# Performance work log

Hardware: AMD Instinct MI355X
Metric: run time of the kernel (lower is better)

## Reference

```python
import jax, jax.numpy as jnp
import numpy as np

NUM_HEADS = 8
GN_GROUPS = 8
GN_EPS = 1e-5


def setup_inputs() -> dict:
    key = jax.random.key(0)
    k1, k2, k3 = jax.random.split(key, 3)
    B, C, H, W = 8, 512, 32, 32
    x = jax.random.normal(k1, (B, C, H, W), dtype=jnp.float32)
    w_qkv = jax.random.normal(k2, (3 * C, C), dtype=jnp.float32) * 0.02
    w_proj = jax.random.normal(k3, (C, C), dtype=jnp.float32) * 0.02
    gamma = jnp.ones((C,), dtype=jnp.float32)
    beta = jnp.zeros((C,), dtype=jnp.float32)
    return {"x": x, "w_qkv": w_qkv, "w_proj": w_proj, "gamma": gamma, "beta": beta}


def reference(x, w_qkv, w_proj, gamma, beta):
    B, C, H, W = x.shape
    nh = NUM_HEADS
    hd = C // nh
    N = H * W
    scale = jnp.asarray(hd, x.dtype) ** -0.5

    xf = x.reshape(B, C, N)                                  # [B,C,N]
    # 1x1 conv (no bias) == channel matmul
    qkv = jnp.einsum('oc,bcn->bon', w_qkv, xf)               # [B,3C,N]
    qkv = qkv.reshape(B, 3, nh, hd, N)
    q, k, v = qkv[:, 0], qkv[:, 1], qkv[:, 2]                # [B,h,d,N]

    attn = jnp.einsum('bhdn,bhdm->bhnm', q, k) * scale       # [B,h,N,N]
    attn = jax.nn.softmax(attn, axis=-1)
    out = jnp.einsum('bhnm,bhdm->bhdn', attn, v)             # [B,h,d,N]
    out = out.reshape(B, C, N)

    out = jnp.einsum('oc,bcn->bon', w_proj, out).reshape(B, C, H, W)

    # GroupNorm(8, C)
    g = GN_GROUPS
    og = out.reshape(B, g, C // g, H, W)
    mean = og.mean(axis=(2, 3, 4), keepdims=True)
    var = og.var(axis=(2, 3, 4), keepdims=True)
    normed = ((og - mean) * jax.lax.rsqrt(var + GN_EPS)).reshape(B, C, H, W)
    normed = normed * gamma[None, :, None, None] + beta[None, :, None, None]

    return normed + x
```

## Files before the change

### kernel.cpp

```cpp
#include <hip/hip_runtime.h>

#define B_DIM 8
#define GN_EPS 1e-5f

typedef short s16x8 __attribute__((ext_vector_type(8)));
typedef float f32x4 __attribute__((ext_vector_type(4)));
typedef unsigned int u32x2 __attribute__((ext_vector_type(2)));
typedef s16x8 s16x8_a __attribute__((may_alias));
typedef u32x2 u32x2_a __attribute__((may_alias));

__device__ inline unsigned short f2bf(float f) {
    unsigned u = __builtin_bit_cast(unsigned, f);
    u += 0x7fffu + ((u >> 16) & 1u);
    return (unsigned short)(u >> 16);
}

__device__ inline unsigned cvtpk(float lo, float hi) {
    unsigned r;
    asm("v_cvt_pk_bf16_f32 %0, %1, %2" : "=v"(r) : "v"(lo), "v"(hi));
    return r;
}

__device__ inline f32x4 mfma16(s16x8 a, s16x8 b, f32x4 c) {
    return __builtin_amdgcn_mfma_f32_16x16x32_bf16(a, b, c, 0, 0, 0);
}

__device__ inline void gload16(const unsigned short* g, unsigned short* l) {
    __builtin_amdgcn_global_load_lds(
        (const __attribute__((address_space(1))) unsigned int*)g,
        (__attribute__((address_space(3))) unsigned int*)l, 16, 0, 0);
}

#define SWZ(r, c) ((r)*64 + ((c) ^ (((r)&7) << 3)))

__global__ __launch_bounds__(256)
void wcvt_kernel(const float4* __restrict__ src, unsigned short* __restrict__ dst) {
    int idx = blockIdx.x * 256 + threadIdx.x;
    float4 v = src[idx];
    ushort4 pk;
    pk.x = f2bf(v.x); pk.y = f2bf(v.y); pk.z = f2bf(v.z); pk.w = f2bf(v.w);
    *(ushort4*)&dst[(size_t)idx * 4] = pk;
}

__global__ __launch_bounds__(256)
void xT_kernel(const float* __restrict__ x, unsigned short* __restrict__ xt) {
    const int ntile = blockIdx.x, ctile = blockIdx.y, b = blockIdx.z;
    const int t = threadIdx.x;
    __shared__ float ts[64][65];
    const float* xp = x + ((size_t)b * 512 + ctile * 64) * 1024 + ntile * 64;
    #pragma unroll
    for (int i = 0; i < 16; ++i) {
        int f = i * 256 + t; int c = f >> 6, n = f & 63;
        ts[n][c] = xp[(size_t)c * 1024 + n];
    }
    __syncthreads();
    unsigned short* xo = xt + ((size_t)b * 1024 + ntile * 64) * 512 + ctile * 64;
    #pragma unroll
    for (int i = 0; i < 16; ++i) {
        int f = i * 256 + t; int n = f >> 6, c = f & 63;
        xo[(size_t)n * 512 + c] = f2bf(ts[n][c]);
    }
}

template<int O_DIM, int MODE>
__global__ __launch_bounds__(256)
void mm_kernel(const unsigned short* __restrict__ Wb,
               const unsigned short* __restrict__ Xt,
               float* __restrict__ Yout,
               unsigned short* __restrict__ qt,
               unsigned short* __restrict__ kt,
               unsigned short* __restrict__ vt) {
    constexpr int OT = O_DIM / 128;
    const int bi = blockIdx.x;
    const int nt = bi & 7;
    const int rest = bi >> 3;
    const int ot = rest % OT;
    const int b  = rest / OT;

    const int t = threadIdx.x;
    const int w = t >> 6, lid = t & 63, lr = lid & 15, g4 = lid >> 4;
    const int wr = w >> 1, wc = w & 1;

    __shared__ unsigned short lds[17408];
    unsigned short* Ws = lds;
    unsigned short* Xs = lds + 4096;

    const unsigned short* wsrc = Wb + ((size_t)(ot * 128 + w * 32 + (lid >> 2))) * 512 + (lid & 3) * 8;
    const unsigned short* xsrc = Xt + ((size_t)b * 1024 + nt * 128 + w * 32 + (lid >> 2)) * 512 + (lid & 3) * 8;
    unsigned short* wdst0 = Ws + (w * 32) * 32;
    unsigned short* wdst1 = Ws + (w * 32 + 16) * 32;
    unsigned short* xdst0 = Xs + (w * 32) * 32;
    unsigned short* xdst1 = Xs + (w * 32 + 16) * 32;

    const f32x4 Z4 = {0.f, 0.f, 0.f, 0.f};
    f32x4 acc[4][4];
    #pragma unroll
    for (int i = 0; i < 4; ++i)
        #pragma unroll
        for (int j = 0; j < 4; ++j) acc[i][j] = Z4;

    #pragma unroll 1
    for (int k0 = 0; k0 < 512; k0 += 32) {
        __syncthreads();
        gload16(wsrc + k0, wdst0);
        gload16(wsrc + k0 + 16 * 512, wdst1);
        gload16(xsrc + k0, xdst0);
        gload16(xsrc + k0 + 16 * 512, xdst1);
        __syncthreads();
        s16x8 av[4], bv[4];
        #pragma unroll
        for (int mi = 0; mi < 4; ++mi)
            av[mi] = *(const s16x8*)&Ws[(wr * 64 + mi * 16 + lr) * 32 + g4 * 8];
        #pragma unroll
        for (int nj = 0; nj < 4; ++nj)
            bv[nj] = *(const s16x8*)&Xs[(wc * 64 + nj * 16 + lr) * 32 + g4 * 8];
        #pragma unroll
        for (int mi = 0; mi < 4; ++mi)
            #pragma unroll
            for (int nj = 0; nj < 4; ++nj)
                acc[mi][nj] = mfma16(av[mi], bv[nj], acc[mi][nj]);
    }

    if (MODE == 0) {
        float* yp = Yout + ((size_t)b * O_DIM + ot * 128 + wr * 64) * 1024 + nt * 128 + wc * 64;
        #pragma unroll
        for (int mi = 0; mi < 4; ++mi)
            #pragma unroll
            for (int nj = 0; nj < 4; ++nj)
                #pragma unroll
                for (int r = 0; r < 4; ++r)
                    yp[(size_t)(mi * 16 + g4 * 4 + r) * 1024 + nj * 16 + lr] = acc[mi][nj][r];
    } else {
        __syncthreads();
        unsigned short* T = lds + w * 4352;
        const int obase = ot * 128 + wr * 64;
        const int s = obase >> 9;
        const int h = (obase >> 6) & 7;
        const float scl = (s == 0) ? 0.18033688f : 1.0f;
        #pragma unroll
        for (int mi = 0; mi < 4; ++mi)
            #pragma unroll
            for (int nj = 0; nj < 4; ++nj)
                #pragma unroll
                for (int r = 0; r < 4; ++r) {
                    int ol = mi * 16 + g4 * 4 + r, nl = nj * 16 + lr;
                    unsigned short v = f2bf(acc[mi][nj][r] * scl);
                    T[(s < 2) ? (nl * 68 + ol) : (ol * 68 + nl)] = v;
                }
        const size_t n0w = (size_t)nt * 128 + wc * 64;
        const int row = (lid >> 5), j = lid & 31;
        if (s < 2) {
            unsigned short* q = (s == 0) ? qt : kt;
            unsigned int* dst = (unsigned int*)(q + (((size_t)b * 8 + h) * 1024 + n0w) * 64);
            #pragma unroll
            for (int p = 0; p < 32; ++p) {
                int rw = p * 2 + row;
                unsigned int lo = T[rw * 68 + 2 * j];
                unsigned int hi = T[rw * 68 + 2 * j + 1];
                dst[(size_t)rw * 32 + j] = lo | (hi << 16);
            }
        } else {
            unsigned int* dst = (unsigned int*)(vt + ((size_t)b * 8 + h) * 65536 + n0w);
            #pragma unroll
            for (int p = 0; p < 32; ++p) {
                int rw = p * 2 + row;
                unsigned int lo = T[rw * 68 + 2 * j];
                unsigned int hi = T[rw * 68 + 2 * j + 1];
                dst[(size_t)rw * 512 + j] = lo | (hi << 16);
            }
        }
    }
}

__global__ __launch_bounds__(256)
void attn_kernel(const unsigned short* __restrict__ qt,
                 const unsigned short* __restrict__ kt,
                 const unsigned short* __restrict__ vt,
                 unsigned short* __restrict__ aout) {
    const int bi = blockIdx.x;
    const int h = bi & 7;
    const int qtile = (bi >> 3) & 7;
    const int b = bi >> 6;

    const int t = threadIdx.x;
    const int w = t >> 6, lid = t & 63, lr = lid & 15, g4 = lid >> 4;
    const int rr = lid >> 3, cc = lid & 7;
    const int csw = (cc ^ rr) << 3;

    __shared__ unsigned short lds[24576];
    unsigned short* Ps = lds + 16384;

    const unsigned short* qbh = qt + ((size_t)b * 8 + h) * 65536;
    const unsigned short* kbh = kt + ((size_t)b * 8 + h) * 65536;
    const unsigned short* vbh = vt + ((size_t)b * 8 + h) * 65536;

    s16x8 qa[2][2];
    #pragma unroll
    for (int mi = 0; mi < 2; ++mi)
        #pragma unroll
        for (int ks = 0; ks < 2; ++ks)
            qa[mi][ks] = *(const s16x8*)(qbh +
                (size_t)(qtile * 128 + w * 32 + mi * 16 + lr) * 64 + ks * 32 + g4 * 8);

    {
        unsigned short* Kd = lds + (w * 16) * 64;
        unsigned short* Vd = lds + 8192 + (w * 16) * 64;
        gload16(kbh + (size_t)(w * 16 + rr) * 64 + csw, Kd);
        gload16(kbh + (size_t)(w * 16 + 8 + rr) * 64 + csw, Kd + 512);
        gload16(vbh + (size_t)(w * 16 + rr) * 1024 + csw, Vd);
        gload16(vbh + (size_t)(w * 16 + 8 + rr) * 1024 + csw, Vd + 512);
    }
    __syncthreads();

    const f32x4 Z4 = {0.f, 0.f, 0.f, 0.f};
    f32x4 acc_o[2][4];
    float l_run[2] = {0.f, 0.f};
    #pragma unroll
    for (int mi = 0; mi < 2; ++mi)
        #pragma unroll
        for (int di = 0; di < 4; ++di) acc_o[mi][di] = Z4;

    #pragma unroll 1
    for (int it = 0; it < 16; ++it) {
        const int sel = it & 1;
        unsigned short* Kc = lds + sel * 4096;
        unsigned short* Vc = lds + 8192 + sel * 4096;

        if (it < 15) {
            const int m1 = (it + 1) * 64;
            unsigned short* Kd = lds + (sel ^ 1) * 4096 + (w * 16) * 64;
            unsigned short* Vd = lds + 8192 + (sel ^ 1) * 4096 + (w * 16) * 64;
            gload16(kbh + (size_t)(m1 + w * 16 + rr) * 64 + csw, Kd);
            gload16(kbh + (size_t)(m1 + w * 16 + 8 + rr) * 64 + csw, Kd + 512);
            gload16(vbh + (size_t)(w * 16 + rr) * 1024 + m1 + csw, Vd);
            gload16(vbh + (size_t)(w * 16 + 8 + rr) * 1024 + m1 + csw, Vd + 512);
        }

        f32x4 sc[2][4];
        #pragma unroll
        for (int mi = 0; mi < 2; ++mi)
            #pragma unroll
            for (int mj = 0; mj < 4; ++mj) sc[mi][mj] = Z4;
        #pragma unroll
        for (int ks = 0; ks < 2; ++ks) {
            s16x8 kb[4];
            #pragma unroll
            for (int mj = 0; mj < 4; ++mj)
                kb[mj] = *(const s16x8*)&Kc[SWZ(mj * 16 + lr, ks * 32 + g4 * 8)];
            #pragma unroll
            for (int mi = 0; mi < 2; ++mi)
                #pragma unroll
                for (int mj = 0; mj < 4; ++mj)
                    sc[mi][mj] = mfma16(kb[mj], qa[mi][ks], sc[mi][mj]);
        }

        #pragma unroll
        for (int mi = 0; mi < 2; ++mi) {
            #pragma unroll
            for (int mj = 0; mj < 4; ++mj) {
                float p0 = __builtin_amdgcn_exp2f(sc[mi][mj][0]);
                float p1 = __builtin_amdgcn_exp2f(sc[mi][mj][1]);
                float p2 = __builtin_amdgcn_exp2f(sc[mi][mj][2]);
                float p3 = __builtin_amdgcn_exp2f(sc[mi][mj][3]);
                l_run[mi] += (p0 + p1) + (p2 + p3);
                u32x2 pk;
                pk.x = cvtpk(p0, p1);
                pk.y = cvtpk(p2, p3);
                *(u32x2_a*)&Ps[SWZ(w * 32 + mi * 16 + lr, mj * 16 + g4 * 4)] = pk;
            }
        }

        #pragma unroll
        for (int ks = 0; ks < 2; ++ks) {
            s16x8 pa[2], vb[4];
            #pragma unroll
            for (int mi = 0; mi < 2; ++mi)
                pa[mi] = *(const s16x8_a*)&Ps[SWZ(w * 32 + mi * 16 + lr, ks * 32 + g4 * 8)];
            #pragma unroll
            for (int di = 0; di < 4; ++di)
                vb[di] = *(const s16x8*)&Vc[SWZ(di * 16 + lr, ks * 32 + g4 * 8)];
            #pragma unroll
            for (int mi = 0; mi < 2; ++mi)
                #pragma unroll
                for (int di = 0; di < 4; ++di)
                    acc_o[mi][di] = mfma16(pa[mi], vb[di], acc_o[mi][di]);
        }
        __syncthreads();
    }

    #pragma unroll
    for (int mi = 0; mi < 2; ++mi) {
        float l = l_run[mi];
        l += __shfl_xor(l, 16);
        l += __shfl_xor(l, 32);
        l_run[mi] = 1.f / l;
    }
    #pragma unroll
    for (int mi = 0; mi < 2; ++mi) {
        float inv[4];
        #pragma unroll
        for (int r = 0; r < 4; ++r)
            inv[r] = __shfl(l_run[mi], g4 * 4 + r);
        #pragma unroll
        for (int di = 0; di < 4; ++di)
            #pragma unroll
            for (int r = 0; r < 4; ++r) {
                int n = qtile * 128 + w * 32 + mi * 16 + g4 * 4 + r;
                int c = h * 64 + di * 16 + lr;
                aout[((size_t)b * 1024 + n) * 512 + c] = f2bf(acc_o[mi][di][r] * inv[r]);
            }
    }
}

__global__ __launch_bounds__(256)
void gn_stats_kernel(const float* __restrict__ proj, float* __restrict__ partial) {
    const int s = blockIdx.x;
    const int g = blockIdx.y;
    const int b = blockIdx.z;
    const int t = threadIdx.x;
    const float4* p4 = (const float4*)(proj + ((size_t)b * 512 + (size_t)g * 64) * 1024)
                       + (size_t)s * 2048;
    float sum = 0.f, sq = 0.f;
    #pragma unroll
    for (int r = 0; r < 8; ++r) {
        float4 v = p4[r * 256 + t];
        sum += v.x + v.y + v.z + v.w;
        sq  += v.x * v.x + v.y * v.y + v.z * v.z + v.w * v.w;
    }
    #pragma unroll
    for (int off = 32; off >= 1; off >>= 1) {
        sum += __shfl_down(sum, off);
        sq  += __shfl_down(sq, off);
    }
    __shared__ float rs[4], rq[4];
    if ((t & 63) == 0) { rs[t >> 6] = sum; rq[t >> 6] = sq; }
    __syncthreads();
    if (t == 0) {
        float* pp = partial + ((size_t)(b * 8 + g) * 8 + s) * 2;
        pp[0] = rs[0] + rs[1] + rs[2] + rs[3];
        pp[1] = rq[0] + rq[1] + rq[2] + rq[3];
    }
}

__global__ __launch_bounds__(256)
void gn_apply_kernel(const float* __restrict__ partial, const float* __restrict__ x,
                     const float* __restrict__ gamma, const float* __restrict__ beta,
                     float* __restrict__ out) {
    const int qtr = blockIdx.x;
    const int g = blockIdx.y;
    const int b = blockIdx.z;
    const int t = threadIdx.x;
    const float* pp = partial + (size_t)(b * 8 + g) * 16;
    float sum = 0.f, sq = 0.f;
    #pragma unroll
    for (int s = 0; s < 8; ++s) { sum += pp[s * 2]; sq += pp[s * 2 + 1]; }
    const float mean = sum * (1.f / 65536.f);
    const float var  = sq * (1.f / 65536.f) - mean * mean;
    const float rstd = rsqrtf(var + GN_EPS);
    const size_t base = ((size_t)b * 512 + (size_t)g * 64) * 1024 + (size_t)qtr * 4096;
    const float4* o4 = (const float4*)(out + base);
    const float4* x4 = (const float4*)(x + base);
    float4* w4 = (float4*)(out + base);
    #pragma unroll
    for (int j = 0; j < 4; ++j) {
        int c = g * 64 + qtr * 4 + j;
        float gm = gamma[c], bt = beta[c];
        float4 v  = o4[j * 256 + t];
        float4 xv = x4[j * 256 + t];
        float4 r;
        r.x = (v.x - mean) * rstd * gm + bt + xv.x;
        r.y = (v.y - mean) * rstd * gm + bt + xv.y;
        r.z = (v.z - mean) * rstd * gm + bt + xv.z;
        r.w = (v.w - mean) * rstd * gm + bt + xv.w;
        w4[j * 256 + t] = r;
    }
}

extern "C" void kernel_launch(void* const* d_in, const int* in_sizes, int n_in,
                              void* d_out, int out_size, void* d_ws, size_t ws_size,
                              hipStream_t stream) {
    (void)in_sizes; (void)n_in; (void)out_size; (void)ws_size;
    const float* x      = (const float*)d_in[0];
    const float* w_qkv  = (const float*)d_in[1];
    const float* w_proj = (const float*)d_in[2];
    const float* gamma  = (const float*)d_in[3];
    const float* beta   = (const float*)d_in[4];
    float* out = (float*)d_out;

    unsigned short* qtb  = (unsigned short*)d_ws;
    unsigned short* ktb  = qtb  + 4194304;
    unsigned short* vtb  = ktb  + 4194304;
    unsigned short* aoutb= vtb  + 4194304;
    unsigned short* xtb  = aoutb+ 4194304;
    unsigned short* wqb  = xtb  + 4194304;
    unsigned short* wpb  = wqb  + 786432;
    float* partial = (float*)(wpb + 262144);

    wcvt_kernel<<<768, 256, 0, stream>>>((const float4*)w_qkv, wqb);
    wcvt_kernel<<<256, 256, 0, stream>>>((const float4*)w_proj, wpb);
    xT_kernel<<<dim3(16, 8, B_DIM), 256, 0, stream>>>(x, xtb);
    mm_kernel<1536, 1><<<768, 256, 0, stream>>>(wqb, xtb, nullptr, qtb, ktb, vtb);
    attn_kernel<<<512, 256, 0, stream>>>(qtb, ktb, vtb, aoutb);
    mm_kernel<512, 0><<<256, 256, 0, stream>>>(wpb, aoutb, out, nullptr, nullptr, nullptr);
    gn_stats_kernel<<<dim3(8, 8, B_DIM), 256, 0, stream>>>(out, partial);
    gn_apply_kernel<<<dim3(16, 8, B_DIM), 256, 0, stream>>>(partial, x, gamma, beta, out);
}
```

Baseline: 91.44 us.

## Fuse GroupNorm stats into projection GEMM and halve attention query tile

The projection GEMM epilogue now computes per-wave sums and sums of squares and writes them as partials, so the separate GroupNorm statistics kernel and its re-read of the projection output are removed. The apply kernel now reduces 16 partials per group instead of 8. Separately, the attention kernel processes 64 query rows per block instead of 128, doubling the grid to 1024 blocks and cutting per-wave registers and LDS. The price is that K/V tiles are loaded twice as often per query row.

```diff
diff --git a/kernel.cpp b/kernel.cpp
--- a/kernel.cpp
+++ b/kernel.cpp
@@ -69,7 +69,8 @@
                float* __restrict__ Yout,
                unsigned short* __restrict__ qt,
                unsigned short* __restrict__ kt,
-               unsigned short* __restrict__ vt) {
+               unsigned short* __restrict__ vt,
+               float* __restrict__ partial) {
     constexpr int OT = O_DIM / 128;
     const int bi = blockIdx.x;
     const int nt = bi & 7;
@@ -121,7 +122,7 @@
                 acc[mi][nj] = mfma16(av[mi], bv[nj], acc[mi][nj]);
     }
 
-    if (MODE == 0) {
+    if (MODE == 0 || MODE == 2) {
         float* yp = Yout + ((size_t)b * O_DIM + ot * 128 + wr * 64) * 1024 + nt * 128 + wc * 64;
         #pragma unroll
         for (int mi = 0; mi < 4; ++mi)
@@ -130,6 +131,29 @@
                 #pragma unroll
                 for (int r = 0; r < 4; ++r)
                     yp[(size_t)(mi * 16 + g4 * 4 + r) * 1024 + nj * 16 + lr] = acc[mi][nj][r];
+        if (MODE == 2) {
+            float s1 = 0.f, s2 = 0.f;
+            #pragma unroll
+            for (int mi = 0; mi < 4; ++mi)
+                #pragma unroll
+                for (int nj = 0; nj < 4; ++nj)
+                    #pragma unroll
+                    for (int r = 0; r < 4; ++r) {
+                        float v = acc[mi][nj][r];
+                        s1 += v;
+                        s2 += v * v;
+                    }
+            #pragma unroll
+            for (int off = 1; off <= 32; off <<= 1) {
+                s1 += __shfl_xor(s1, off);
+                s2 += __shfl_xor(s2, off);
+            }
+            if (lid == 0) {
+                float2* pp = (float2*)partial + ((size_t)(b * 8 + ot * 2 + wr) * 16)
+                             + nt * 2 + wc;
+                *pp = make_float2(s1, s2);
+            }
+        }
     } else {
         __syncthreads();
         unsigned short* T = lds + w * 4352;
@@ -179,28 +203,26 @@
                  unsigned short* __restrict__ aout) {
     const int bi = blockIdx.x;
     const int h = bi & 7;
-    const int qtile = (bi >> 3) & 7;
-    const int b = bi >> 6;
+    const int qtile = (bi >> 3) & 15;
+    const int b = bi >> 7;
 
     const int t = threadIdx.x;
     const int w = t >> 6, lid = t & 63, lr = lid & 15, g4 = lid >> 4;
     const int rr = lid >> 3, cc = lid & 7;
     const int csw = (cc ^ rr) << 3;
 
-    __shared__ unsigned short lds[24576];
+    __shared__ unsigned short lds[20480];
     unsigned short* Ps = lds + 16384;
 
     const unsigned short* qbh = qt + ((size_t)b * 8 + h) * 65536;
     const unsigned short* kbh = kt + ((size_t)b * 8 + h) * 65536;
     const unsigned short* vbh = vt + ((size_t)b * 8 + h) * 65536;
 
-    s16x8 qa[2][2];
-    #pragma unroll
-    for (int mi = 0; mi < 2; ++mi)
-        #pragma unroll
-        for (int ks = 0; ks < 2; ++ks)
-            qa[mi][ks] = *(const s16x8*)(qbh +
-                (size_t)(qtile * 128 + w * 32 + mi * 16 + lr) * 64 + ks * 32 + g4 * 8);
+    s16x8 qa[2];
+    #pragma unroll
+    for (int ks = 0; ks < 2; ++ks)
+        qa[ks] = *(const s16x8*)(qbh +
+            (size_t)(qtile * 64 + w * 16 + lr) * 64 + ks * 32 + g4 * 8);
 
     {
         unsigned short* Kd = lds + (w * 16) * 64;
@@ -213,12 +235,10 @@
     __syncthreads();
 
     const f32x4 Z4 = {0.f, 0.f, 0.f, 0.f};
-    f32x4 acc_o[2][4];
-    float l_run[2] = {0.f, 0.f};
-    #pragma unroll
-    for (int mi = 0; mi < 2; ++mi)
-        #pragma unroll
-        for (int di = 0; di < 4; ++di) acc_o[mi][di] = Z4;
+    f32x4 acc_o[4];
+    float l_run = 0.f;
+    #pragma unroll
+    for (int di = 0; di < 4; ++di) acc_o[di] = Z4;
 
     #pragma unroll 1
     for (int it = 0; it < 16; ++it) {
@@ -236,11 +256,9 @@
             gload16(vbh + (size_t)(w * 16 + 8 + rr) * 1024 + m1 + csw, Vd + 512);
         }
 
-        f32x4 sc[2][4];
-        #pragma unroll
-        for (int mi = 0; mi < 2; ++mi)
-            #pragma unroll
-            for (int mj = 0; mj < 4; ++mj) sc[mi][mj] = Z4;
+        f32x4 sc[4];
+        #pragma unroll
+        for (int mj = 0; mj < 4; ++mj) sc[mj] = Z4;
         #pragma unroll
         for (int ks = 0; ks < 2; ++ks) {
             s16x8 kb[4];
@@ -248,98 +266,52 @@
             for (int mj = 0; mj < 4; ++mj)
                 kb[mj] = *(const s16x8*)&Kc[SWZ(mj * 16 + lr, ks * 32 + g4 * 8)];
             #pragma unroll
-            for (int mi = 0; mi < 2; ++mi)
-                #pragma unroll
-                for (int mj = 0; mj < 4; ++mj)
-                    sc[mi][mj] = mfma16(kb[mj], qa[mi][ks], sc[mi][mj]);
-        }
-
-        #pragma unroll
-        for (int mi = 0; mi < 2; ++mi) {
-            #pragma unroll
-            for (int mj = 0; mj < 4; ++mj) {
-                float p0 = __builtin_amdgcn_exp2f(sc[mi][mj][0]);
-                float p1 = __builtin_amdgcn_exp2f(sc[mi][mj][1]);
-                float p2 = __builtin_amdgcn_exp2f(sc[mi][mj][2]);
-                float p3 = __builtin_amdgcn_exp2f(sc[mi][mj][3]);
-                l_run[mi] += (p0 + p1) + (p2 + p3);
-                u32x2 pk;
-                pk.x = cvtpk(p0, p1);
-                pk.y = cvtpk(p2, p3);
-                *(u32x2_a*)&Ps[SWZ(w * 32 + mi * 16 + lr, mj * 16 + g4 * 4)] = pk;
-            }
+            for (int mj = 0; mj < 4; ++mj)
+                sc[mj] = mfma16(kb[mj], qa[ks], sc[mj]);
+        }
+
+        #pragma unroll
+        for (int mj = 0; mj < 4; ++mj) {
+            float p0 = __builtin_amdgcn_exp2f(sc[mj][0]);
+            float p1 = __builtin_amdgcn_exp2f(sc[mj][1]);
+            float p2 = __builtin_amdgcn_exp2f(sc[mj][2]);
+            float p3 = __builtin_amdgcn_exp2f(sc[mj][3]);
+            l_run += (p0 + p1) + (p2 + p3);
+            u32x2 pk;
+            pk.x = cvtpk(p0, p1);
+            pk.y = cvtpk(p2, p3);
+            *(u32x2_a*)&Ps[SWZ(w * 16 + lr, mj * 16 + g4 * 4)] = pk;
         }
 
         #pragma unroll
         for (int ks = 0; ks < 2; ++ks) {
-            s16x8 pa[2], vb[4];
-            #pragma unroll
-            for (int mi = 0; mi < 2; ++mi)
-                pa[mi] = *(const s16x8_a*)&Ps[SWZ(w * 32 + mi * 16 + lr, ks * 32 + g4 * 8)];
+            s16x8 pa, vb[4];
+            pa = *(const s16x8_a*)&Ps[SWZ(w * 16 + lr, ks * 32 + g4 * 8)];
             #pragma unroll
             for (int di = 0; di < 4; ++di)
                 vb[di] = *(const s16x8*)&Vc[SWZ(di * 16 + lr, ks * 32 + g4 * 8)];
             #pragma unroll
-            for (int mi = 0; mi < 2; ++mi)
-                #pragma unroll
-                for (int di = 0; di < 4; ++di)
-                    acc_o[mi][di] = mfma16(pa[mi], vb[di], acc_o[mi][di]);
+            for (int di = 0; di < 4; ++di)
+                acc_o[di] = mfma16(pa, vb[di], acc_o[di]);
         }
         __syncthreads();
     }
 
-    #pragma unroll
-    for (int mi = 0; mi < 2; ++mi) {
-        float l = l_run[mi];
-        l += __shfl_xor(l, 16);
-        l += __shfl_xor(l, 32);
-        l_run[mi] = 1.f / l;
-    }
-    #pragma unroll
-    for (int mi = 0; mi < 2; ++mi) {
-        float inv[4];
-        #pragma unroll
-        for (int r = 0; r < 4; ++r)
-            inv[r] = __shfl(l_run[mi], g4 * 4 + r);
-        #pragma unroll
-        for (int di = 0; di < 4; ++di)
-            #pragma unroll
-            for (int r = 0; r < 4; ++r) {
-                int n = qtile * 128 + w * 32 + mi * 16 + g4 * 4 + r;
-                int c = h * 64 + di * 16 + lr;
-                aout[((size_t)b * 1024 + n) * 512 + c] = f2bf(acc_o[mi][di][r] * inv[r]);
-            }
-    }
-}
-
-__global__ __launch_bounds__(256)
-void gn_stats_kernel(const float* __restrict__ proj, float* __restrict__ partial) {
-    const int s = blockIdx.x;
-    const int g = blockIdx.y;
-    const int b = blockIdx.z;
-    const int t = threadIdx.x;
-    const float4* p4 = (const float4*)(proj + ((size_t)b * 512 + (size_t)g * 64) * 1024)
-                       + (size_t)s * 2048;
-    float sum = 0.f, sq = 0.f;
-    #pragma unroll
-    for (int r = 0; r < 8; ++r) {
-        float4 v = p4[r * 256 + t];
-        sum += v.x + v.y + v.z + v.w;
-        sq  += v.x * v.x + v.y * v.y + v.z * v.z + v.w * v.w;
-    }
-    #pragma unroll
-    for (int off = 32; off >= 1; off >>= 1) {
-        sum += __shfl_down(sum, off);
-        sq  += __shfl_down(sq, off);
-    }
-    __shared__ float rs[4], rq[4];
-    if ((t & 63) == 0) { rs[t >> 6] = sum; rq[t >> 6] = sq; }
-    __syncthreads();
-    if (t == 0) {
-        float* pp = partial + ((size_t)(b * 8 + g) * 8 + s) * 2;
-        pp[0] = rs[0] + rs[1] + rs[2] + rs[3];
-        pp[1] = rq[0] + rq[1] + rq[2] + rq[3];
-    }
+    l_run += __shfl_xor(l_run, 16);
+    l_run += __shfl_xor(l_run, 32);
+    l_run = 1.f / l_run;
+    float inv[4];
+    #pragma unroll
+    for (int r = 0; r < 4; ++r)
+        inv[r] = __shfl(l_run, g4 * 4 + r);
+    #pragma unroll
+    for (int di = 0; di < 4; ++di)
+        #pragma unroll
+        for (int r = 0; r < 4; ++r) {
+            int n = qtile * 64 + w * 16 + g4 * 4 + r;
+            int c = h * 64 + di * 16 + lr;
+            aout[((size_t)b * 1024 + n) * 512 + c] = f2bf(acc_o[di][r] * inv[r]);
+        }
 }
 
 __global__ __launch_bounds__(256)
@@ -350,10 +322,10 @@
     const int g = blockIdx.y;
     const int b = blockIdx.z;
     const int t = threadIdx.x;
-    const float* pp = partial + (size_t)(b * 8 + g) * 16;
+    const float2* pp = (const float2*)partial + (size_t)(b * 8 + g) * 16;
     float sum = 0.f, sq = 0.f;
     #pragma unroll
-    for (int s = 0; s < 8; ++s) { sum += pp[s * 2]; sq += pp[s * 2 + 1]; }
+    for (int s = 0; s < 16; ++s) { sum += pp[s].x; sq += pp[s].y; }
     const float mean = sum * (1.f / 65536.f);
     const float var  = sq * (1.f / 65536.f) - mean * mean;
     const float rstd = rsqrtf(var + GN_EPS);
@@ -399,9 +371,8 @@
     wcvt_kernel<<<768, 256, 0, stream>>>((const float4*)w_qkv, wqb);
     wcvt_kernel<<<256, 256, 0, stream>>>((const float4*)w_proj, wpb);
     xT_kernel<<<dim3(16, 8, B_DIM), 256, 0, stream>>>(x, xtb);
-    mm_kernel<1536, 1><<<768, 256, 0, stream>>>(wqb, xtb, nullptr, qtb, ktb, vtb);
-    attn_kernel<<<512, 256, 0, stream>>>(qtb, ktb, vtb, aoutb);
-    mm_kernel<512, 0><<<256, 256, 0, stream>>>(wpb, aoutb, out, nullptr, nullptr, nullptr);
-    gn_stats_kernel<<<dim3(8, 8, B_DIM), 256, 0, stream>>>(out, partial);
+    mm_kernel<1536, 1><<<768, 256, 0, stream>>>(wqb, xtb, nullptr, qtb, ktb, vtb, nullptr);
+    attn_kernel<<<1024, 256, 0, stream>>>(qtb, ktb, vtb, aoutb);
+    mm_kernel<512, 2><<<256, 256, 0, stream>>>(wpb, aoutb, out, nullptr, nullptr, nullptr, partial);
     gn_apply_kernel<<<dim3(16, 8, B_DIM), 256, 0, stream>>>(partial, x, gamma, beta, out);
 }
```

Measured after the change: 90.83 us. No clear change (-0.7%).

## Double-buffer GEMM K-loop, fuse GroupNorm stats into proj GEMM, pack xT stores

Applied to the files above, without the earlier changes.

The GEMM main loop now double-buffers its LDS tiles, prefetching the next K slice while the current one feeds the MFMAs, which halves the barriers per iteration. The projection GEMM gets a new mode that reduces per-wave sum and sum-of-squares from the accumulators and writes partials, so the separate gn_stats kernel and its re-read of the output are removed. The apply kernel now reads 16 partials per group. The transpose kernel also writes two bf16 values per 32-bit store.

```diff
diff --git a/kernel.cpp b/kernel.cpp
--- a/kernel.cpp
+++ b/kernel.cpp
@@ -56,9 +56,11 @@
     __syncthreads();
     unsigned short* xo = xt + ((size_t)b * 1024 + ntile * 64) * 512 + ctile * 64;
     #pragma unroll
-    for (int i = 0; i < 16; ++i) {
-        int f = i * 256 + t; int n = f >> 6, c = f & 63;
-        xo[(size_t)n * 512 + c] = f2bf(ts[n][c]);
+    for (int i = 0; i < 8; ++i) {
+        int f = i * 512 + t * 2; int n = f >> 6, c = f & 63;
+        unsigned lo = f2bf(ts[n][c]);
+        unsigned hi = f2bf(ts[n][c + 1]);
+        *(unsigned int*)&xo[(size_t)n * 512 + c] = lo | (hi << 16);
     }
 }
 
@@ -69,7 +71,8 @@
                float* __restrict__ Yout,
                unsigned short* __restrict__ qt,
                unsigned short* __restrict__ kt,
-               unsigned short* __restrict__ vt) {
+               unsigned short* __restrict__ vt,
+               float* __restrict__ partial) {
     constexpr int OT = O_DIM / 128;
     const int bi = blockIdx.x;
     const int nt = bi & 7;
@@ -82,15 +85,11 @@
     const int wr = w >> 1, wc = w & 1;
 
     __shared__ unsigned short lds[17408];
-    unsigned short* Ws = lds;
-    unsigned short* Xs = lds + 4096;
 
     const unsigned short* wsrc = Wb + ((size_t)(ot * 128 + w * 32 + (lid >> 2))) * 512 + (lid & 3) * 8;
     const unsigned short* xsrc = Xt + ((size_t)b * 1024 + nt * 128 + w * 32 + (lid >> 2)) * 512 + (lid & 3) * 8;
-    unsigned short* wdst0 = Ws + (w * 32) * 32;
-    unsigned short* wdst1 = Ws + (w * 32 + 16) * 32;
-    unsigned short* xdst0 = Xs + (w * 32) * 32;
-    unsigned short* xdst1 = Xs + (w * 32 + 16) * 32;
+    const int woff0 = (w * 32) * 32;
+    const int woff1 = (w * 32 + 16) * 32;
 
     const f32x4 Z4 = {0.f, 0.f, 0.f, 0.f};
     f32x4 acc[4][4];
@@ -99,29 +98,40 @@
         #pragma unroll
         for (int j = 0; j < 4; ++j) acc[i][j] = Z4;
 
+    gload16(wsrc, lds + woff0);
+    gload16(wsrc + 16 * 512, lds + woff1);
+    gload16(xsrc, lds + 4096 + woff0);
+    gload16(xsrc + 16 * 512, lds + 4096 + woff1);
+    __syncthreads();
+
     #pragma unroll 1
-    for (int k0 = 0; k0 < 512; k0 += 32) {
-        __syncthreads();
-        gload16(wsrc + k0, wdst0);
-        gload16(wsrc + k0 + 16 * 512, wdst1);
-        gload16(xsrc + k0, xdst0);
-        gload16(xsrc + k0 + 16 * 512, xdst1);
-        __syncthreads();
+    for (int it = 0; it < 16; ++it) {
+        const int sel = it & 1;
+        unsigned short* buf = lds + sel * 8192;
+        if (it < 15) {
+            const int k1 = (it + 1) * 32;
+            unsigned short* nb = lds + (sel ^ 1) * 8192;
+            gload16(wsrc + k1, nb + woff0);
+            gload16(wsrc + k1 + 16 * 512, nb + woff1);
+            gload16(xsrc + k1, nb + 4096 + woff0);
+            gload16(xsrc + k1 + 16 * 512, nb + 4096 + woff1);
+        }
         s16x8 av[4], bv[4];
         #pragma unroll
         for (int mi = 0; mi < 4; ++mi)
-            av[mi] = *(const s16x8*)&Ws[(wr * 64 + mi * 16 + lr) * 32 + g4 * 8];
+            av[mi] = *(const s16x8*)&buf[(wr * 64 + mi * 16 + lr) * 32 + g4 * 8];
         #pragma unroll
         for (int nj = 0; nj < 4; ++nj)
-            bv[nj] = *(const s16x8*)&Xs[(wc * 64 + nj * 16 + lr) * 32 + g4 * 8];
+            bv[nj] = *(const s16x8*)&buf[4096 + (wc * 64 + nj * 16 + lr) * 32 + g4 * 8];
         #pragma unroll
         for (int mi = 0; mi < 4; ++mi)
             #pragma unroll
             for (int nj = 0; nj < 4; ++nj)
                 acc[mi][nj] = mfma16(av[mi], bv[nj], acc[mi][nj]);
-    }
-
-    if (MODE == 0) {
+        __syncthreads();
+    }
+
+    if (MODE == 0 || MODE == 2) {
         float* yp = Yout + ((size_t)b * O_DIM + ot * 128 + wr * 64) * 1024 + nt * 128 + wc * 64;
         #pragma unroll
         for (int mi = 0; mi < 4; ++mi)
@@ -130,8 +140,30 @@
                 #pragma unroll
                 for (int r = 0; r < 4; ++r)
                     yp[(size_t)(mi * 16 + g4 * 4 + r) * 1024 + nj * 16 + lr] = acc[mi][nj][r];
+        if (MODE == 2) {
+            float s1 = 0.f, s2 = 0.f;
+            #pragma unroll
+            for (int mi = 0; mi < 4; ++mi)
+                #pragma unroll
+                for (int nj = 0; nj < 4; ++nj)
+                    #pragma unroll
+                    for (int r = 0; r < 4; ++r) {
+                        float v = acc[mi][nj][r];
+                        s1 += v;
+                        s2 += v * v;
+                    }
+            #pragma unroll
+            for (int off = 1; off <= 32; off <<= 1) {
+                s1 += __shfl_xor(s1, off);
+                s2 += __shfl_xor(s2, off);
+            }
+            if (lid == 0) {
+                float2* pp = (float2*)partial + ((size_t)(b * 8 + ot * 2 + wr) * 16)
+                             + nt * 2 + wc;
+                *pp = make_float2(s1, s2);
+            }
+        }
     } else {
-        __syncthreads();
         unsigned short* T = lds + w * 4352;
         const int obase = ot * 128 + wr * 64;
         const int s = obase >> 9;
@@ -313,36 +345,6 @@
 }
 
 __global__ __launch_bounds__(256)
-void gn_stats_kernel(const float* __restrict__ proj, float* __restrict__ partial) {
-    const int s = blockIdx.x;
-    const int g = blockIdx.y;
-    const int b = blockIdx.z;
-    const int t = threadIdx.x;
-    const float4* p4 = (const float4*)(proj + ((size_t)b * 512 + (size_t)g * 64) * 1024)
-                       + (size_t)s * 2048;
-    float sum = 0.f, sq = 0.f;
-    #pragma unroll
-    for (int r = 0; r < 8; ++r) {
-        float4 v = p4[r * 256 + t];
-        sum += v.x + v.y + v.z + v.w;
-        sq  += v.x * v.x + v.y * v.y + v.z * v.z + v.w * v.w;
-    }
-    #pragma unroll
-    for (int off = 32; off >= 1; off >>= 1) {
-        sum += __shfl_down(sum, off);
-        sq  += __shfl_down(sq, off);
-    }
-    __shared__ float rs[4], rq[4];
-    if ((t & 63) == 0) { rs[t >> 6] = sum; rq[t >> 6] = sq; }
-    __syncthreads();
-    if (t == 0) {
-        float* pp = partial + ((size_t)(b * 8 + g) * 8 + s) * 2;
-        pp[0] = rs[0] + rs[1] + rs[2] + rs[3];
-        pp[1] = rq[0] + rq[1] + rq[2] + rq[3];
-    }
-}
-
-__global__ __launch_bounds__(256)
 void gn_apply_kernel(const float* __restrict__ partial, const float* __restrict__ x,
                      const float* __restrict__ gamma, const float* __restrict__ beta,
                      float* __restrict__ out) {
@@ -350,10 +352,10 @@
     const int g = blockIdx.y;
     const int b = blockIdx.z;
     const int t = threadIdx.x;
-    const float* pp = partial + (size_t)(b * 8 + g) * 16;
+    const float2* pp = (const float2*)partial + (size_t)(b * 8 + g) * 16;
     float sum = 0.f, sq = 0.f;
     #pragma unroll
-    for (int s = 0; s < 8; ++s) { sum += pp[s * 2]; sq += pp[s * 2 + 1]; }
+    for (int s = 0; s < 16; ++s) { sum += pp[s].x; sq += pp[s].y; }
     const float mean = sum * (1.f / 65536.f);
     const float var  = sq * (1.f / 65536.f) - mean * mean;
     const float rstd = rsqrtf(var + GN_EPS);
@@ -399,9 +401,8 @@
     wcvt_kernel<<<768, 256, 0, stream>>>((const float4*)w_qkv, wqb);
     wcvt_kernel<<<256, 256, 0, stream>>>((const float4*)w_proj, wpb);
     xT_kernel<<<dim3(16, 8, B_DIM), 256, 0, stream>>>(x, xtb);
-    mm_kernel<1536, 1><<<768, 256, 0, stream>>>(wqb, xtb, nullptr, qtb, ktb, vtb);
+    mm_kernel<1536, 1><<<768, 256, 0, stream>>>(wqb, xtb, nullptr, qtb, ktb, vtb, nullptr);
     attn_kernel<<<512, 256, 0, stream>>>(qtb, ktb, vtb, aoutb);
-    mm_kernel<512, 0><<<256, 256, 0, stream>>>(wpb, aoutb, out, nullptr, nullptr, nullptr);
-    gn_stats_kernel<<<dim3(8, 8, B_DIM), 256, 0, stream>>>(out, partial);
+    mm_kernel<512, 2><<<256, 256, 0, stream>>>(wpb, aoutb, out, nullptr, nullptr, nullptr, partial);
     gn_apply_kernel<<<dim3(16, 8, B_DIM), 256, 0, stream>>>(partial, x, gamma, beta, out);
 }
```

Result: faster. 83.76 us (-8.4%).
